# Kernel optimization log

Hardware: AMD Instinct MI355X
Metric: run time of the kernel (lower is better)

Reference implementation:

```python
import jax, jax.numpy as jnp
import numpy as np

N = 50000      # nodes
E = 800000     # edges
IN = 128       # in_dim
H = 64         # h_dim
OUT = 64       # out_dim
R = 5          # num_relations
TB = 12        # 4 * BINS


def setup_inputs() -> dict:
    key = jax.random.key(0)
    ks = jax.random.split(key, 20)
    x = jax.random.normal(ks[0], (N, IN), jnp.float32)
    edge_index = jax.random.randint(ks[1], (2, E), 0, N)
    edge_type = jax.random.randint(ks[2], (E,), 0, R)
    edge_time = jax.random.uniform(ks[3], (E, TB), jnp.float32)
    # xavier_normal on (1,1) -> std 1; on (12,1) -> std sqrt(2/13)
    lambda_sym = jax.random.normal(ks[4], (), jnp.float32)
    beta = jax.random.normal(ks[5], (TB, 1), jnp.float32) * np.float32(np.sqrt(2.0 / (TB + 1)))
    def lin(k, fan_in, fan_out):
        kw, kb = jax.random.split(k)
        bound = 1.0 / np.sqrt(fan_in)
        W = jax.random.uniform(kw, (fan_in, fan_out), jnp.float32, -bound, bound)
        b = jax.random.uniform(kb, (fan_out,), jnp.float32, -bound, bound)
        return W, b
    field_W, field_b = lin(ks[6], IN, H)
    r1 = [lin(k, 2 * H, H) for k in jax.random.split(ks[7], R)]
    r2 = [lin(k, 2 * H, H) for k in jax.random.split(ks[8], R)]
    rel1_W = jnp.stack([w for w, _ in r1]); rel1_b = jnp.stack([b for _, b in r1])
    rel2_W = jnp.stack([w for w, _ in r2]); rel2_b = jnp.stack([b for _, b in r2])
    out0_W, out0_b = lin(ks[9], H, OUT)
    out1_W, out1_b = lin(ks[10], H, OUT)
    out2_W, out2_b = lin(ks[11], H, OUT)
    return {"x": x, "edge_index": edge_index, "edge_type": edge_type, "edge_time": edge_time,
            "lambda_sym": lambda_sym, "beta": beta, "field_W": field_W, "field_b": field_b,
            "rel1_W": rel1_W, "rel1_b": rel1_b, "rel2_W": rel2_W, "rel2_b": rel2_b,
            "out0_W": out0_W, "out0_b": out0_b, "out1_W": out1_W, "out1_b": out1_b,
            "out2_W": out2_W, "out2_b": out2_b}


def _geo_layer(x_emb, src, dst, edge_type, edge_time, lambda_sym, beta, relW, relb):
    # PyG source_to_target: x_j = x[src], x_i = x[dst]; sum-aggregate into dst.
    x_j = x_emb[src]                       # [E, H] gather
    x_i = x_emb[dst]                       # [E, H] gather
    edge_x = jnp.concatenate([x_j, x_i], axis=-1)  # [E, 2H]
    # logit = sum of 4 blockwise dot-products == edge_time @ beta
    logit = (edge_time @ beta)[:, 0]       # [E]
    w = lambda_sym * jnp.exp(-logit)       # [E] time-decay weight
    # relation-specific linear, selected by edge_type (masks partition edges)
    msg = jnp.zeros((edge_x.shape[0], relW.shape[-1]), dtype=x_emb.dtype)
    for r in range(R):
        mask = (edge_type == r)[:, None]
        msg = msg + jnp.where(mask, edge_x @ relW[r] + relb[r], 0.0)
    msg = w[:, None] * msg
    return jax.ops.segment_sum(msg, dst, num_segments=x_emb.shape[0])


def reference(x, edge_index, edge_type, edge_time, lambda_sym, beta,
              field_W, field_b, rel1_W, rel1_b, rel2_W, rel2_b,
              out0_W, out0_b, out1_W, out1_b, out2_W, out2_b):
    src, dst = edge_index[0], edge_index[1]
    e0 = x @ field_W + field_b
    e1 = _geo_layer(e0, src, dst, edge_type, edge_time, lambda_sym, beta, rel1_W, rel1_b)
    e2 = _geo_layer(e1, src, dst, edge_type, edge_time, lambda_sym, beta, rel2_W, rel2_b)
    lr = jax.nn.leaky_relu  # negative_slope 0.01, same as torch default
    return lr(e2 @ out2_W + out2_b) + lr(e1 @ out1_W + out1_b) + lr(e0 @ out0_W + out0_b)
```

## Files before the change

### kernel.cpp

```cpp
#include <hip/hip_runtime.h>
#include <cstdint>
#include <cstddef>

#define NN 50000
#define NE 800000
#define RREL 5
#define NR (NN * RREL)
#define NB5 ((NR + 255) / 256)

typedef __attribute__((ext_vector_type(8))) short short8;
typedef __attribute__((ext_vector_type(4))) float f32x4;
typedef unsigned short ushort_t;

static __device__ __forceinline__ float lrelu(float v) { return v > 0.f ? v : 0.01f * v; }

static __device__ __forceinline__ unsigned short f32_bf16_rn(float x) {
    unsigned u = __float_as_uint(x);
    return (unsigned short)((u + 0x7FFFu + ((u >> 16) & 1u)) >> 16);
}
static __device__ __forceinline__ float bf16_f32(unsigned short h) {
    return __uint_as_float(((unsigned)h) << 16);
}

static __device__ __forceinline__ void split8v(float4 q0, float4 q1, short8& hi, short8& lo) {
    float v[8] = {q0.x, q0.y, q0.z, q0.w, q1.x, q1.y, q1.z, q1.w};
    #pragma unroll
    for (int j = 0; j < 8; ++j) {
        unsigned short h = f32_bf16_rn(v[j]);
        float hf = __uint_as_float(((unsigned)h) << 16);
        unsigned short l = f32_bf16_rn(v[j] - hf);
        hi[j] = (short)h; lo[j] = (short)l;
    }
}

static __device__ __forceinline__ short8 zero8() {
    short8 z = {0, 0, 0, 0, 0, 0, 0, 0};
    return z;
}

__launch_bounds__(256)
__global__ void zero_deg5(int4* __restrict__ p, int n4)
{
    int i = blockIdx.x * 256 + threadIdx.x;
    int stride = gridDim.x * 256;
    for (; i < n4; i += stride)
        p[i] = make_int4(0, 0, 0, 0);
}

__launch_bounds__(512)
__global__ void lin_mfma(const float* __restrict__ X,
                         const short8* __restrict__ ff,
                         const float* __restrict__ bias,
                         ushort_t* __restrict__ Cb, int M)
{
    __shared__ short8 wl[16 * 64];

    const int t = threadIdx.x;
    const int wid = t >> 6, lane = t & 63;
    const int lc = lane & 15, lg = lane >> 4;
    const int row0 = blockIdx.x * 128 + wid * 16;

    const int nA = row0 + lc;
    const bool okA = (nA < M);
    const int nodeA = okA ? nA : 0;

    wl[t] = ff[t];
    wl[t + 512] = ff[t + 512];

    short8 ah[4], al[4];
    #pragma unroll
    for (int s = 0; s < 4; ++s) {
        const float* p = &X[(size_t)nodeA * 128 + s * 32 + lg * 8];
        float4 q0 = okA ? *(const float4*)p       : make_float4(0,0,0,0);
        float4 q1 = okA ? *(const float4*)(p + 4) : make_float4(0,0,0,0);
        split8v(q0, q1, ah[s], al[s]);
    }
    __syncthreads();

    f32x4 acc[4];
    #pragma unroll
    for (int nf = 0; nf < 4; ++nf) acc[nf] = (f32x4){0.f, 0.f, 0.f, 0.f};

    #pragma unroll
    for (int s = 0; s < 4; ++s)
        #pragma unroll
        for (int nf = 0; nf < 4; ++nf) {
            short8 bh = wl[(s * 4 + nf) * 64 + lane];
            acc[nf] = __builtin_amdgcn_mfma_f32_16x16x32_bf16(ah[s], bh, acc[nf], 0, 0, 0);
            acc[nf] = __builtin_amdgcn_mfma_f32_16x16x32_bf16(al[s], bh, acc[nf], 0, 0, 0);
        }

    float bb[4];
    #pragma unroll
    for (int nf = 0; nf < 4; ++nf) bb[nf] = bias[nf * 16 + lc];

    #pragma unroll
    for (int i = 0; i < 4; ++i) {
        int nd = row0 + lg * 4 + i;
        if (nd >= M) continue;
        #pragma unroll
        for (int nf = 0; nf < 4; ++nf)
            Cb[(size_t)nd * 64 + nf * 16 + lc] = f32_bf16_rn(acc[nf][i] + bb[nf]);
    }
}

__launch_bounds__(512)
__global__ void head_mfma(const ushort_t* __restrict__ E0, const ushort_t* __restrict__ E1,
                          const ushort_t* __restrict__ E2,
                          const short8* __restrict__ hf,
                          const float* __restrict__ b0, const float* __restrict__ b1,
                          const float* __restrict__ b2,
                          float* __restrict__ out, int M)
{
    __shared__ short8 wl[24 * 64];

    const int t = threadIdx.x;
    const int wid = t >> 6, lane = t & 63;
    const int lc = lane & 15, lg = lane >> 4;
    const int row0 = blockIdx.x * 128 + wid * 16;

    const int nA = row0 + lc;
    const bool okA = (nA < M);
    const int nodeA = okA ? nA : 0;

    wl[t] = hf[t];
    wl[t + 512] = hf[t + 512];
    wl[t + 1024] = hf[t + 1024];

    const ushort_t* Es[3] = {E0, E1, E2};
    const float* bs[3] = {b0, b1, b2};

    float facc[4][4] = {};
    __syncthreads();

    #pragma unroll
    for (int src = 0; src < 3; ++src) {
        short8 ah[2];
        #pragma unroll
        for (int s = 0; s < 2; ++s) {
            const ushort_t* p = &Es[src][(size_t)nodeA * 64 + s * 32 + lg * 8];
            ah[s] = okA ? *(const short8*)p : zero8();
        }
        f32x4 acc[4];
        #pragma unroll
        for (int nf = 0; nf < 4; ++nf) acc[nf] = (f32x4){0.f, 0.f, 0.f, 0.f};
        #pragma unroll
        for (int s = 0; s < 2; ++s)
            #pragma unroll
            for (int nf = 0; nf < 4; ++nf) {
                short8 bh = wl[((src * 2 + s) * 4 + nf) * 64 + lane];
                acc[nf] = __builtin_amdgcn_mfma_f32_16x16x32_bf16(ah[s], bh, acc[nf], 0, 0, 0);
            }
        float bb[4];
        #pragma unroll
        for (int nf = 0; nf < 4; ++nf) bb[nf] = bs[src][nf * 16 + lc];
        #pragma unroll
        for (int nf = 0; nf < 4; ++nf)
            #pragma unroll
            for (int i = 0; i < 4; ++i)
                facc[nf][i] += lrelu(acc[nf][i] + bb[nf]);
    }

    #pragma unroll
    for (int i = 0; i < 4; ++i) {
        int nd = row0 + lg * 4 + i;
        if (nd >= M) continue;
        #pragma unroll
        for (int nf = 0; nf < 4; ++nf)
            out[(size_t)nd * 64 + nf * 16 + lc] = facc[nf][i];
    }
}

__launch_bounds__(256)
__global__ void zgather(const int* __restrict__ offs5,
                        const unsigned long long* __restrict__ epack,
                        const ushort_t* __restrict__ Eb,
                        ushort_t* __restrict__ Zb16, float* __restrict__ S)
{
    int wid = (blockIdx.x * 256 + threadIdx.x) >> 6;
    int lane = threadIdx.x & 63;
    if (wid >= NN) return;
    const int b = wid * RREL;

    int p    = __builtin_amdgcn_readfirstlane(offs5[b]);
    int n1   = __builtin_amdgcn_readfirstlane(offs5[b + 1]);
    int n2   = __builtin_amdgcn_readfirstlane(offs5[b + 2]);
    int n3   = __builtin_amdgcn_readfirstlane(offs5[b + 3]);
    int n4   = __builtin_amdgcn_readfirstlane(offs5[b + 4]);
    int pend = __builtin_amdgcn_readfirstlane(offs5[b + 5]);

    ushort_t* zr = Zb16 + (size_t)wid * 320 + lane;
    const int INFP = 0x7fffffff;

    int r = 0;
    float zA = 0.f, zB = 0.f, zC = 0.f, zD = 0.f;
    float sA = 0.f, sB = 0.f, sC = 0.f, sD = 0.f;

#define WVAL(q) __uint_as_float((unsigned)((q) >> 32))
#define SRCI(q) ((unsigned)(q) & 0xFFFFFFFFu)

#define FLUSH_CHECK(pe)                                                     \
    while (r < 4 && (pe) == n1) {                                           \
        zr[(size_t)(r << 6)] = f32_bf16_rn(zA + zB + zC + zD);              \
        if (lane == 0) S[b + r] = sA + sB + sC + sD;                        \
        zA = zB = zC = zD = 0.f; sA = sB = sC = sD = 0.f;                   \
        ++r; n1 = n2; n2 = n3; n3 = n4; n4 = INFP;                          \
    }

    for (; p + 8 <= pend; p += 8) {
        unsigned long long q0 = epack[p + 0];
        unsigned long long q1 = epack[p + 1];
        unsigned long long q2 = epack[p + 2];
        unsigned long long q3 = epack[p + 3];
        unsigned long long q4 = epack[p + 4];
        unsigned long long q5 = epack[p + 5];
        unsigned long long q6 = epack[p + 6];
        unsigned long long q7 = epack[p + 7];
        float v0 = bf16_f32(Eb[(size_t)SRCI(q0) * 64 + lane]);
        float v1 = bf16_f32(Eb[(size_t)SRCI(q1) * 64 + lane]);
        float v2 = bf16_f32(Eb[(size_t)SRCI(q2) * 64 + lane]);
        float v3 = bf16_f32(Eb[(size_t)SRCI(q3) * 64 + lane]);
        float v4 = bf16_f32(Eb[(size_t)SRCI(q4) * 64 + lane]);
        float v5 = bf16_f32(Eb[(size_t)SRCI(q5) * 64 + lane]);
        float v6 = bf16_f32(Eb[(size_t)SRCI(q6) * 64 + lane]);
        float v7 = bf16_f32(Eb[(size_t)SRCI(q7) * 64 + lane]);

        FLUSH_CHECK(p + 0);
        zA = fmaf(WVAL(q0), v0, zA); sA += WVAL(q0);
        FLUSH_CHECK(p + 1);
        zB = fmaf(WVAL(q1), v1, zB); sB += WVAL(q1);
        FLUSH_CHECK(p + 2);
        zC = fmaf(WVAL(q2), v2, zC); sC += WVAL(q2);
        FLUSH_CHECK(p + 3);
        zD = fmaf(WVAL(q3), v3, zD); sD += WVAL(q3);
        FLUSH_CHECK(p + 4);
        zA = fmaf(WVAL(q4), v4, zA); sA += WVAL(q4);
        FLUSH_CHECK(p + 5);
        zB = fmaf(WVAL(q5), v5, zB); sB += WVAL(q5);
        FLUSH_CHECK(p + 6);
        zC = fmaf(WVAL(q6), v6, zC); sC += WVAL(q6);
        FLUSH_CHECK(p + 7);
        zD = fmaf(WVAL(q7), v7, zD); sD += WVAL(q7);
    }
    for (; p < pend; ++p) {
        unsigned long long q = epack[p];
        float v = bf16_f32(Eb[(size_t)SRCI(q) * 64 + lane]);
        FLUSH_CHECK(p);
        zA = fmaf(WVAL(q), v, zA);
        sA += WVAL(q);
    }
    while (r < RREL) {
        zr[(size_t)(r << 6)] = f32_bf16_rn(zA + zB + zC + zD);
        if (lane == 0) S[b + r] = sA + sB + sC + sD;
        zA = zB = zC = zD = 0.f; sA = sB = sC = sD = 0.f;
        ++r;
    }
#undef FLUSH_CHECK
#undef WVAL
#undef SRCI
}

__launch_bounds__(256)
__global__ void prep_wfrag(const float* __restrict__ rel1_W, const float* __restrict__ rel2_W,
                           const float* __restrict__ field_W,
                           const float* __restrict__ out0_W, const float* __restrict__ out1_W,
                           const float* __restrict__ out2_W,
                           short8* __restrict__ wf1, short8* __restrict__ wf2,
                           short8* __restrict__ ff, short8* __restrict__ hf)
{
    int bid = blockIdx.x;
    int t = threadIdx.x;

    if (bid < 20) {
        int layer = bid / 10, c = bid % 10;
        const float* relW = layer ? rel2_W : rel1_W;
        short8* wf = layer ? wf2 : wf1;
        for (int sl = t; sl < 512; sl += 256) {
            int rid = sl >> 6, lane = sl & 63;
            int s = rid >> 2, nf = rid & 3;
            int g = lane >> 4, lc = lane & 15;
            int r = (c < 5) ? c : c - 5;
            const float* W = relW + (size_t)r * 8192 + ((c < 5) ? 0 : 4096);
            float v[8];
            #pragma unroll
            for (int j = 0; j < 8; ++j)
                v[j] = W[(size_t)(s * 32 + g * 8 + j) * 64 + nf * 16 + lc];
            float4 q0 = make_float4(v[0], v[1], v[2], v[3]);
            float4 q1 = make_float4(v[4], v[5], v[6], v[7]);
            short8 hi, lo;
            split8v(q0, q1, hi, lo);
            size_t slot = (size_t)c * 1024 + (size_t)((s * 4 + nf) * 64 + lane) * 2;
            wf[slot]     = hi;
            wf[slot + 1] = lo;
        }
    } else if (bid < 24) {
        int s = bid - 20;
        for (int sl = t; sl < 256; sl += 256) {
            int nf = sl >> 6, lane = sl & 63;
            int g = lane >> 4, lc = lane & 15;
            float v[8];
            #pragma unroll
            for (int j = 0; j < 8; ++j)
                v[j] = field_W[(size_t)(s * 32 + g * 8 + j) * 64 + nf * 16 + lc];
            short8 hi;
            #pragma unroll
            for (int j = 0; j < 8; ++j) hi[j] = (short)f32_bf16_rn(v[j]);
            ff[(size_t)(s * 4 + nf) * 64 + lane] = hi;
        }
    } else {
        int hsrc = bid - 24;
        const float* W = (hsrc == 0) ? out0_W : (hsrc == 1) ? out1_W : out2_W;
        for (int sl = t; sl < 512; sl += 256) {
            int rid = sl >> 6, lane = sl & 63;
            int s = rid >> 2, nf = rid & 3;
            if (s >= 2) continue;
            int g = lane >> 4, lc = lane & 15;
            float v[8];
            #pragma unroll
            for (int j = 0; j < 8; ++j)
                v[j] = W[(size_t)(s * 32 + g * 8 + j) * 64 + nf * 16 + lc];
            short8 hi;
            #pragma unroll
            for (int j = 0; j < 8; ++j) hi[j] = (short)f32_bf16_rn(v[j]);
            hf[(size_t)((hsrc * 2 + s) * 4 + nf) * 64 + lane] = hi;
        }
    }
}

__launch_bounds__(512)
__global__ void zgemm_mfma(const ushort_t* __restrict__ Zb16,
                           const ushort_t* __restrict__ EbPrev,
                           const short8* __restrict__ wf,
                           const float* __restrict__ relb,
                           const float* __restrict__ S,
                           ushort_t* __restrict__ Enb, int M)
{
    __shared__ short8 wlds[2][1024];

    const int t = threadIdx.x;
    const int wid = t >> 6, lane = t & 63;
    const int lc = lane & 15, lg = lane >> 4;
    const int row0 = blockIdx.x * 128 + wid * 16;

    const int nA = row0 + lc;
    const bool okA = (nA < M);
    const int nodeA = okA ? nA : 0;

    const int sq = t >> 6, sl = t & 63;
    const int wrA = (sq * 2 + 0) * 64 + sl;
    const int wrB = (sq * 2 + 1) * 64 + sl;

    short8 eh[2];
    #pragma unroll
    for (int s = 0; s < 2; ++s) {
        const ushort_t* p = &EbPrev[(size_t)nodeA * 64 + s * 32 + lg * 8];
        eh[s] = okA ? *(const short8*)p : zero8();
    }

    float sD[4][RREL];
    #pragma unroll
    for (int i = 0; i < 4; ++i) {
        int nd = row0 + lg * 4 + i;
        int ns = (nd < M) ? nd : 0;
        #pragma unroll
        for (int r = 0; r < RREL; ++r)
            sD[i][r] = S[(size_t)ns * RREL + r];
    }

    {
        const short8* wp = wf + (size_t)t * 2;
        short8 sa = wp[0], sb = wp[1];
        wlds[0][wrA] = sa; wlds[0][wrB] = sb;
    }
    short8 az0, az1;
    {
        const ushort_t* zb = &Zb16[(size_t)nodeA * 320 + lg * 8];
        az0 = okA ? *(const short8*)(zb)      : zero8();
        az1 = okA ? *(const short8*)(zb + 32) : zero8();
    }
    __syncthreads();

    f32x4 acc[4];
    #pragma unroll
    for (int nf = 0; nf < 4; ++nf) acc[nf] = (f32x4){0.f, 0.f, 0.f, 0.f};

    short8 sreg_a, sreg_b;
    short8 pz0, pz1;

    #pragma unroll
    for (int c = 0; c < 10; ++c) {
        const int cb = c & 1;
        if (c < 9) {
            const short8* wp = wf + (size_t)(c + 1) * 1024 + (size_t)t * 2;
            sreg_a = wp[0]; sreg_b = wp[1];
        }
        if (c < 4) {
            const ushort_t* zb = &Zb16[(size_t)nodeA * 320 + (c + 1) * 64 + lg * 8];
            pz0 = okA ? *(const short8*)(zb)      : zero8();
            pz1 = okA ? *(const short8*)(zb + 32) : zero8();
        }

        if (c < 5) {
            #pragma unroll
            for (int s = 0; s < 2; ++s) {
                short8 Az = (s == 0) ? az0 : az1;
                #pragma unroll
                for (int nf = 0; nf < 4; ++nf) {
                    short8 bh = wlds[cb][((s * 4 + nf) * 2 + 0) * 64 + lane];
                    short8 bl = wlds[cb][((s * 4 + nf) * 2 + 1) * 64 + lane];
                    acc[nf] = __builtin_amdgcn_mfma_f32_16x16x32_bf16(Az, bh, acc[nf], 0, 0, 0);
                    acc[nf] = __builtin_amdgcn_mfma_f32_16x16x32_bf16(Az, bl, acc[nf], 0, 0, 0);
                }
            }
        } else {
            f32x4 tmp[4];
            #pragma unroll
            for (int nf = 0; nf < 4; ++nf) tmp[nf] = (f32x4){0.f, 0.f, 0.f, 0.f};
            #pragma unroll
            for (int s = 0; s < 2; ++s)
                #pragma unroll
                for (int nf = 0; nf < 4; ++nf) {
                    short8 bh = wlds[cb][((s * 4 + nf) * 2 + 0) * 64 + lane];
                    short8 bl = wlds[cb][((s * 4 + nf) * 2 + 1) * 64 + lane];
                    tmp[nf] = __builtin_amdgcn_mfma_f32_16x16x32_bf16(eh[s], bh, tmp[nf], 0, 0, 0);
                    tmp[nf] = __builtin_amdgcn_mfma_f32_16x16x32_bf16(eh[s], bl, tmp[nf], 0, 0, 0);
                }
            const int r = c - 5;
            #pragma unroll
            for (int nf = 0; nf < 4; ++nf)
                #pragma unroll
                for (int i = 0; i < 4; ++i)
                    acc[nf][i] += sD[i][r] * tmp[nf][i];
        }

        if (c < 4) { az0 = pz0; az1 = pz1; }

        if (c < 9) {
            __syncthreads();
            wlds[cb ^ 1][wrA] = sreg_a;
            wlds[cb ^ 1][wrB] = sreg_b;
            __syncthreads();
        }
    }

    float bbv[4][RREL];
    #pragma unroll
    for (int nf = 0; nf < 4; ++nf)
        #pragma unroll
        for (int r = 0; r < RREL; ++r)
            bbv[nf][r] = relb[r * 64 + nf * 16 + lc];

    #pragma unroll
    for (int i = 0; i < 4; ++i) {
        int nd = row0 + lg * 4 + i;
        if (nd >= M) continue;
        #pragma unroll
        for (int nf = 0; nf < 4; ++nf) {
            float v = acc[nf][i];
            #pragma unroll
            for (int r = 0; r < RREL; ++r)
                v += sD[i][r] * bbv[nf][r];
            Enb[(size_t)nd * 64 + nf * 16 + lc] = f32_bf16_rn(v);
        }
    }
}

__launch_bounds__(256)
__global__ void deg5_hist(const int* __restrict__ dst, const int* __restrict__ etype,
                          int* __restrict__ deg5, int* __restrict__ slot5)
{
    int e = blockIdx.x * 256 + threadIdx.x;
    if (e < NE) slot5[e] = atomicAdd(&deg5[dst[e] * RREL + etype[e]], 1);
}

__launch_bounds__(256)
__global__ void b1_reduce(const int* __restrict__ deg5, int* __restrict__ b1)
{
    __shared__ int sh[256];
    int i = blockIdx.x * 256 + threadIdx.x;
    sh[threadIdx.x] = (i < NR) ? deg5[i] : 0;
    __syncthreads();
    for (int s = 128; s > 0; s >>= 1) {
        if (threadIdx.x < s) sh[threadIdx.x] += sh[threadIdx.x + s];
        __syncthreads();
    }
    if (threadIdx.x == 0) b1[blockIdx.x] = sh[0];
}

__launch_bounds__(256)
__global__ void scan_seq(int* __restrict__ b1, int n)
{
    __shared__ int sh[256];
    __shared__ int carry;
    if (threadIdx.x == 0) carry = 0;
    __syncthreads();
    for (int base = 0; base < n; base += 256) {
        int i = base + threadIdx.x;
        int v = (i < n) ? b1[i] : 0;
        sh[threadIdx.x] = v;
        __syncthreads();
        for (int off = 1; off < 256; off <<= 1) {
            int x = (threadIdx.x >= off) ? sh[threadIdx.x - off] : 0;
            __syncthreads();
            sh[threadIdx.x] += x;
            __syncthreads();
        }
        int excl = sh[threadIdx.x] - v + carry;
        if (i < n) b1[i] = excl;
        __syncthreads();
        if (threadIdx.x == 255) carry = excl + v;
        __syncthreads();
    }
}

__launch_bounds__(256)
__global__ void offs5_final(const int* __restrict__ deg5, const int* __restrict__ b1,
                            int* __restrict__ offs5)
{
    __shared__ int sh[256];
    int t = threadIdx.x;
    int i = blockIdx.x * 256 + t;
    int v = (i < NR) ? deg5[i] : 0;
    sh[t] = v;
    __syncthreads();
    for (int off = 1; off < 256; off <<= 1) {
        int x = (t >= off) ? sh[t - off] : 0;
        __syncthreads();
        sh[t] += x;
        __syncthreads();
    }
    int excl = sh[t] - v + b1[blockIdx.x];
    if (i <= NR) offs5[i] = excl;
}

__launch_bounds__(256)
__global__ void scatter_pass(const int* __restrict__ src, const int* __restrict__ dst,
                             const int* __restrict__ etype,
                             const float* __restrict__ etime,
                             const float* __restrict__ beta,
                             const float* __restrict__ lambda_p,
                             const int* __restrict__ slot5, const int* __restrict__ offs5,
                             unsigned long long* __restrict__ epack)
{
    int e = blockIdx.x * 256 + threadIdx.x;
    if (e >= NE) return;
    float b[12];
    #pragma unroll
    for (int j = 0; j < 12; ++j) b[j] = beta[j];
    const float* et = etime + (size_t)e * 12;
    float4 v0 = *(const float4*)(et);
    float4 v1 = *(const float4*)(et + 4);
    float4 v2 = *(const float4*)(et + 8);
    float logit = v0.x*b[0] + v0.y*b[1] + v0.z*b[2] + v0.w*b[3]
                + v1.x*b[4] + v1.y*b[5] + v1.z*b[6] + v1.w*b[7]
                + v2.x*b[8] + v2.y*b[9] + v2.z*b[10] + v2.w*b[11];
    float we = lambda_p[0] * expf(-logit);
    int p = offs5[dst[e] * RREL + etype[e]] + slot5[e];
    epack[p] = ((unsigned long long)__float_as_uint(we) << 32) | (unsigned)src[e];
}

extern "C" void kernel_launch(void* const* d_in, const int* in_sizes, int n_in,
                              void* d_out, int out_size, void* d_ws, size_t ws_size,
                              hipStream_t stream)
{
    const float* x        = (const float*)d_in[0];
    const int*   eidx     = (const int*)d_in[1];
    const int*   etype    = (const int*)d_in[2];
    const float* etime    = (const float*)d_in[3];
    const float* lambda_p = (const float*)d_in[4];
    const float* beta     = (const float*)d_in[5];
    const float* field_W  = (const float*)d_in[6];
    const float* field_b  = (const float*)d_in[7];
    const float* rel1_W   = (const float*)d_in[8];
    const float* rel1_b   = (const float*)d_in[9];
    const float* rel2_W   = (const float*)d_in[10];
    const float* rel2_b   = (const float*)d_in[11];
    const float* out0_W   = (const float*)d_in[12];
    const float* out0_b   = (const float*)d_in[13];
    const float* out1_W   = (const float*)d_in[14];
    const float* out1_b   = (const float*)d_in[15];
    const float* out2_W   = (const float*)d_in[16];
    const float* out2_b   = (const float*)d_in[17];
    const int* src = eidx;
    const int* dst = eidx + NE;
    float* out = (float*)d_out;

    char* wsb = (char*)d_ws;
    size_t off = 0;
    auto carve = [&](size_t bytes) -> void* {
        void* p = (void*)(wsb + off);
        off += (bytes + 255) & ~(size_t)255;
        return p;
    };
    int*   deg5   = (int*)carve((size_t)NR * 4);
    int*   offs5  = (int*)carve((size_t)(NR + 1) * 4);
    int*   b1     = (int*)carve((size_t)NB5 * 4);
    int*   slot5  = (int*)carve((size_t)NE * 4);
    float* S      = (float*)carve((size_t)NR * 4);
    unsigned long long* epack = (unsigned long long*)carve((size_t)NE * 8);
    ushort_t* e0b = (ushort_t*)carve((size_t)NN * 64 * 2);
    ushort_t* e1b = (ushort_t*)carve((size_t)NN * 64 * 2);
    ushort_t* e2b = (ushort_t*)carve((size_t)NN * 64 * 2);
    ushort_t* Zb16 = (ushort_t*)carve((size_t)NN * 320 * 2);
    short8* wf1   = (short8*)carve((size_t)20 * 16384);
    short8* wf2   = (short8*)carve((size_t)20 * 16384);
    short8* ff    = (short8*)carve((size_t)16 * 64 * 16);
    short8* hf    = (short8*)carve((size_t)24 * 64 * 16);

    dim3 blk(256);
    const int NT128 = (NN + 127) / 128;
    const int EB = (NE + 255) / 256;
    const int GB = (NN * 64 + 255) / 256;

    zero_deg5<<<256, blk, 0, stream>>>((int4*)deg5, (NR + 3) / 4);
    deg5_hist<<<EB, blk, 0, stream>>>(dst, etype, deg5, slot5);
    prep_wfrag<<<27, blk, 0, stream>>>(rel1_W, rel2_W, field_W, out0_W, out1_W, out2_W,
                                       wf1, wf2, ff, hf);
    b1_reduce<<<NB5, blk, 0, stream>>>(deg5, b1);
    scan_seq<<<1, blk, 0, stream>>>(b1, NB5);
    offs5_final<<<NB5, blk, 0, stream>>>(deg5, b1, offs5);
    scatter_pass<<<EB, blk, 0, stream>>>(src, dst, etype, etime, beta, lambda_p,
                                         slot5, offs5, epack);

    lin_mfma<<<dim3(NT128), dim3(512), 0, stream>>>(x, ff, field_b, e0b, NN);

    zgather<<<GB, blk, 0, stream>>>(offs5, epack, e0b, Zb16, S);
    zgemm_mfma<<<dim3(NT128), dim3(512), 0, stream>>>(Zb16, e0b, wf1, rel1_b, S, e1b, NN);

    zgather<<<GB, blk, 0, stream>>>(offs5, epack, e1b, Zb16, S);
    zgemm_mfma<<<dim3(NT128), dim3(512), 0, stream>>>(Zb16, e1b, wf2, rel2_b, S, e2b, NN);

    head_mfma<<<dim3(NT128), dim3(512), 0, stream>>>(e0b, e1b, e2b, hf,
                                                     out0_b, out1_b, out2_b, out, NN);
}
```

Measured before the change: 204.0 us.

## Process two edges per wave in zgather with half-wave bf16x2 gathers

Each (node, relation) segment in the CSR is padded to an even length, and the pad slot is filled with a zero-weight dummy edge. zgather can then have each 32-lane half-wave handle a different edge, reading a packed bf16 pair per lane as a 32-bit load. Partial sums from the two halves are combined with a cross-half shuffle before the store. This halves the loop iterations and makes the row gathers wider. The cost is extra shuffles at every flush, somewhat more padded edges, and a changed scan and offset layout.

```diff
diff --git a/kernel.cpp b/kernel.cpp
--- a/kernel.cpp
+++ b/kernel.cpp
@@ -7,6 +7,7 @@
 #define RREL 5
 #define NR (NN * RREL)
 #define NB5 ((NR + 255) / 256)
+#define NEPAD (NE + NR)
 
 typedef __attribute__((ext_vector_type(8))) short short8;
 typedef __attribute__((ext_vector_type(4))) float f32x4;
@@ -181,6 +182,8 @@
     int lane = threadIdx.x & 63;
     if (wid >= NN) return;
     const int b = wid * RREL;
+    const int h = lane >> 5;
+    const int fl = lane & 31;
 
     int p    = __builtin_amdgcn_readfirstlane(offs5[b]);
     int n1   = __builtin_amdgcn_readfirstlane(offs5[b + 1]);
@@ -189,75 +192,71 @@
     int n4   = __builtin_amdgcn_readfirstlane(offs5[b + 4]);
     int pend = __builtin_amdgcn_readfirstlane(offs5[b + 5]);
 
-    ushort_t* zr = Zb16 + (size_t)wid * 320 + lane;
+    const unsigned* Ebu = (const unsigned*)Eb;
+    unsigned* Zu = (unsigned*)Zb16;
     const int INFP = 0x7fffffff;
 
     int r = 0;
-    float zA = 0.f, zB = 0.f, zC = 0.f, zD = 0.f;
-    float sA = 0.f, sB = 0.f, sC = 0.f, sD = 0.f;
-
-#define WVAL(q) __uint_as_float((unsigned)((q) >> 32))
-#define SRCI(q) ((unsigned)(q) & 0xFFFFFFFFu)
+    float z0 = 0.f, z1 = 0.f, sw = 0.f;
 
 #define FLUSH_CHECK(pe)                                                     \
     while (r < 4 && (pe) == n1) {                                           \
-        zr[(size_t)(r << 6)] = f32_bf16_rn(zA + zB + zC + zD);              \
-        if (lane == 0) S[b + r] = sA + sB + sC + sD;                        \
-        zA = zB = zC = zD = 0.f; sA = sB = sC = sD = 0.f;                   \
+        float o0 = z0 + __shfl_xor(z0, 32);                                 \
+        float o1 = z1 + __shfl_xor(z1, 32);                                 \
+        float os = sw + __shfl_xor(sw, 32);                                 \
+        if (h == 0)                                                         \
+            Zu[(size_t)(b + r) * 32 + fl] =                                 \
+                ((unsigned)f32_bf16_rn(o1) << 16) | f32_bf16_rn(o0);        \
+        if (lane == 0) S[b + r] = os;                                       \
+        z0 = z1 = sw = 0.f;                                                 \
         ++r; n1 = n2; n2 = n3; n3 = n4; n4 = INFP;                          \
     }
 
+#define DO_PAIR(q)                                                          \
+    {                                                                       \
+        unsigned srcn = (unsigned)(q);                                      \
+        float w = __uint_as_float((unsigned)((q) >> 32));                   \
+        unsigned fv = Ebu[(size_t)srcn * 32 + fl];                          \
+        float flo = __uint_as_float(fv << 16);                              \
+        float fhi = __uint_as_float(fv & 0xFFFF0000u);                      \
+        z0 = fmaf(w, flo, z0);                                              \
+        z1 = fmaf(w, fhi, z1);                                              \
+        sw += w;                                                            \
+    }
+
     for (; p + 8 <= pend; p += 8) {
-        unsigned long long q0 = epack[p + 0];
-        unsigned long long q1 = epack[p + 1];
-        unsigned long long q2 = epack[p + 2];
-        unsigned long long q3 = epack[p + 3];
-        unsigned long long q4 = epack[p + 4];
-        unsigned long long q5 = epack[p + 5];
-        unsigned long long q6 = epack[p + 6];
-        unsigned long long q7 = epack[p + 7];
-        float v0 = bf16_f32(Eb[(size_t)SRCI(q0) * 64 + lane]);
-        float v1 = bf16_f32(Eb[(size_t)SRCI(q1) * 64 + lane]);
-        float v2 = bf16_f32(Eb[(size_t)SRCI(q2) * 64 + lane]);
-        float v3 = bf16_f32(Eb[(size_t)SRCI(q3) * 64 + lane]);
-        float v4 = bf16_f32(Eb[(size_t)SRCI(q4) * 64 + lane]);
-        float v5 = bf16_f32(Eb[(size_t)SRCI(q5) * 64 + lane]);
-        float v6 = bf16_f32(Eb[(size_t)SRCI(q6) * 64 + lane]);
-        float v7 = bf16_f32(Eb[(size_t)SRCI(q7) * 64 + lane]);
+        unsigned long long q0 = epack[p + 0 + h];
+        unsigned long long q1 = epack[p + 2 + h];
+        unsigned long long q2 = epack[p + 4 + h];
+        unsigned long long q3 = epack[p + 6 + h];
 
         FLUSH_CHECK(p + 0);
-        zA = fmaf(WVAL(q0), v0, zA); sA += WVAL(q0);
-        FLUSH_CHECK(p + 1);
-        zB = fmaf(WVAL(q1), v1, zB); sB += WVAL(q1);
+        DO_PAIR(q0);
         FLUSH_CHECK(p + 2);
-        zC = fmaf(WVAL(q2), v2, zC); sC += WVAL(q2);
-        FLUSH_CHECK(p + 3);
-        zD = fmaf(WVAL(q3), v3, zD); sD += WVAL(q3);
+        DO_PAIR(q1);
         FLUSH_CHECK(p + 4);
-        zA = fmaf(WVAL(q4), v4, zA); sA += WVAL(q4);
-        FLUSH_CHECK(p + 5);
-        zB = fmaf(WVAL(q5), v5, zB); sB += WVAL(q5);
+        DO_PAIR(q2);
         FLUSH_CHECK(p + 6);
-        zC = fmaf(WVAL(q6), v6, zC); sC += WVAL(q6);
-        FLUSH_CHECK(p + 7);
-        zD = fmaf(WVAL(q7), v7, zD); sD += WVAL(q7);
-    }
-    for (; p < pend; ++p) {
-        unsigned long long q = epack[p];
-        float v = bf16_f32(Eb[(size_t)SRCI(q) * 64 + lane]);
+        DO_PAIR(q3);
+    }
+    for (; p < pend; p += 2) {
+        unsigned long long q = epack[p + h];
         FLUSH_CHECK(p);
-        zA = fmaf(WVAL(q), v, zA);
-        sA += WVAL(q);
+        DO_PAIR(q);
     }
     while (r < RREL) {
-        zr[(size_t)(r << 6)] = f32_bf16_rn(zA + zB + zC + zD);
-        if (lane == 0) S[b + r] = sA + sB + sC + sD;
-        zA = zB = zC = zD = 0.f; sA = sB = sC = sD = 0.f;
+        float o0 = z0 + __shfl_xor(z0, 32);
+        float o1 = z1 + __shfl_xor(z1, 32);
+        float os = sw + __shfl_xor(sw, 32);
+        if (h == 0)
+            Zu[(size_t)(b + r) * 32 + fl] =
+                ((unsigned)f32_bf16_rn(o1) << 16) | f32_bf16_rn(o0);
+        if (lane == 0) S[b + r] = os;
+        z0 = z1 = sw = 0.f;
         ++r;
     }
 #undef FLUSH_CHECK
-#undef WVAL
-#undef SRCI
+#undef DO_PAIR
 }
 
 __launch_bounds__(256)
@@ -478,7 +477,8 @@
 {
     __shared__ int sh[256];
     int i = blockIdx.x * 256 + threadIdx.x;
-    sh[threadIdx.x] = (i < NR) ? deg5[i] : 0;
+    int d = (i < NR) ? deg5[i] : 0;
+    sh[threadIdx.x] = (d + 1) & ~1;
     __syncthreads();
     for (int s = 128; s > 0; s >>= 1) {
         if (threadIdx.x < s) sh[threadIdx.x] += sh[threadIdx.x + s];
@@ -515,12 +515,13 @@
 
 __launch_bounds__(256)
 __global__ void offs5_final(const int* __restrict__ deg5, const int* __restrict__ b1,
-                            int* __restrict__ offs5)
+                            int* __restrict__ offs5, unsigned long long* __restrict__ epack)
 {
     __shared__ int sh[256];
     int t = threadIdx.x;
     int i = blockIdx.x * 256 + t;
-    int v = (i < NR) ? deg5[i] : 0;
+    int d = (i < NR) ? deg5[i] : 0;
+    int v = (d + 1) & ~1;
     sh[t] = v;
     __syncthreads();
     for (int off = 1; off < 256; off <<= 1) {
@@ -531,6 +532,7 @@
     }
     int excl = sh[t] - v + b1[blockIdx.x];
     if (i <= NR) offs5[i] = excl;
+    if (i < NR && (d & 1)) epack[excl + d] = 0ULL;
 }
 
 __launch_bounds__(256)
@@ -597,7 +599,7 @@
     int*   b1     = (int*)carve((size_t)NB5 * 4);
     int*   slot5  = (int*)carve((size_t)NE * 4);
     float* S      = (float*)carve((size_t)NR * 4);
-    unsigned long long* epack = (unsigned long long*)carve((size_t)NE * 8);
+    unsigned long long* epack = (unsigned long long*)carve((size_t)NEPAD * 8);
     ushort_t* e0b = (ushort_t*)carve((size_t)NN * 64 * 2);
     ushort_t* e1b = (ushort_t*)carve((size_t)NN * 64 * 2);
     ushort_t* e2b = (ushort_t*)carve((size_t)NN * 64 * 2);
@@ -618,7 +620,7 @@
                                        wf1, wf2, ff, hf);
     b1_reduce<<<NB5, blk, 0, stream>>>(deg5, b1);
     scan_seq<<<1, blk, 0, stream>>>(b1, NB5);
-    offs5_final<<<NB5, blk, 0, stream>>>(deg5, b1, offs5);
+    offs5_final<<<NB5, blk, 0, stream>>>(deg5, b1, offs5, epack);
     scatter_pass<<<EB, blk, 0, stream>>>(src, dst, etype, etime, beta, lambda_p,
                                          slot5, offs5, epack);
 
```

Result: slower. 223.8 us (+9.7%).

## Process two nodes per wavefront in zgather with packed bf16x2 loads

Applied to the files above, without the earlier changes.

Each wavefront now handles two destination nodes, with each half-wave of 32 lanes loading a 32-bit word (two bf16 features) per gathered row instead of one 16-bit value per lane. This halves the number of wavefronts and widens the per-lane gather loads, reducing load instruction count and per-edge overhead. Per-node offsets are no longer wave-uniform (readfirstlane removed), so control flow in the flush loop can diverge between the two halves. Fewer independent accumulators per feature may add some FMA latency.

```diff
diff --git a/kernel.cpp b/kernel.cpp
--- a/kernel.cpp
+++ b/kernel.cpp
@@ -177,34 +177,54 @@
                         const ushort_t* __restrict__ Eb,
                         ushort_t* __restrict__ Zb16, float* __restrict__ S)
 {
-    int wid = (blockIdx.x * 256 + threadIdx.x) >> 6;
+    int gw = (blockIdx.x * 256 + threadIdx.x) >> 6;
     int lane = threadIdx.x & 63;
-    if (wid >= NN) return;
-    const int b = wid * RREL;
-
-    int p    = __builtin_amdgcn_readfirstlane(offs5[b]);
-    int n1   = __builtin_amdgcn_readfirstlane(offs5[b + 1]);
-    int n2   = __builtin_amdgcn_readfirstlane(offs5[b + 2]);
-    int n3   = __builtin_amdgcn_readfirstlane(offs5[b + 3]);
-    int n4   = __builtin_amdgcn_readfirstlane(offs5[b + 4]);
-    int pend = __builtin_amdgcn_readfirstlane(offs5[b + 5]);
-
-    ushort_t* zr = Zb16 + (size_t)wid * 320 + lane;
+    const int h = lane >> 5;
+    const int fl = lane & 31;
+    int node = gw * 2 + h;
+    if (node >= NN) return;
+    const int b = node * RREL;
+
+    int p    = offs5[b];
+    int n1   = offs5[b + 1];
+    int n2   = offs5[b + 2];
+    int n3   = offs5[b + 3];
+    int n4   = offs5[b + 4];
+    int pend = offs5[b + 5];
+
+    const unsigned* Ebu = (const unsigned*)Eb;
+    unsigned* Zu = (unsigned*)Zb16;
     const int INFP = 0x7fffffff;
 
     int r = 0;
-    float zA = 0.f, zB = 0.f, zC = 0.f, zD = 0.f;
-    float sA = 0.f, sB = 0.f, sC = 0.f, sD = 0.f;
-
+    float zA0 = 0.f, zA1 = 0.f, zB0 = 0.f, zB1 = 0.f;
+    float swA = 0.f, swB = 0.f;
+
+#define SRCI(q) ((unsigned)(q))
 #define WVAL(q) __uint_as_float((unsigned)((q) >> 32))
-#define SRCI(q) ((unsigned)(q) & 0xFFFFFFFFu)
 
 #define FLUSH_CHECK(pe)                                                     \
     while (r < 4 && (pe) == n1) {                                           \
-        zr[(size_t)(r << 6)] = f32_bf16_rn(zA + zB + zC + zD);              \
-        if (lane == 0) S[b + r] = sA + sB + sC + sD;                        \
-        zA = zB = zC = zD = 0.f; sA = sB = sC = sD = 0.f;                   \
+        Zu[(size_t)(b + r) * 32 + fl] =                                     \
+            ((unsigned)f32_bf16_rn(zA1 + zB1) << 16) | f32_bf16_rn(zA0 + zB0); \
+        if (fl == 0) S[b + r] = swA + swB;                                  \
+        zA0 = zA1 = zB0 = zB1 = 0.f; swA = swB = 0.f;                       \
         ++r; n1 = n2; n2 = n3; n3 = n4; n4 = INFP;                          \
+    }
+
+#define ACC_A(q, fv)                                                        \
+    {                                                                       \
+        float w = WVAL(q);                                                  \
+        zA0 = fmaf(w, __uint_as_float((fv) << 16), zA0);                    \
+        zA1 = fmaf(w, __uint_as_float((fv) & 0xFFFF0000u), zA1);            \
+        swA += w;                                                           \
+    }
+#define ACC_B(q, fv)                                                        \
+    {                                                                       \
+        float w = WVAL(q);                                                  \
+        zB0 = fmaf(w, __uint_as_float((fv) << 16), zB0);                    \
+        zB1 = fmaf(w, __uint_as_float((fv) & 0xFFFF0000u), zB1);            \
+        swB += w;                                                           \
     }
 
     for (; p + 8 <= pend; p += 8) {
@@ -216,48 +236,42 @@
         unsigned long long q5 = epack[p + 5];
         unsigned long long q6 = epack[p + 6];
         unsigned long long q7 = epack[p + 7];
-        float v0 = bf16_f32(Eb[(size_t)SRCI(q0) * 64 + lane]);
-        float v1 = bf16_f32(Eb[(size_t)SRCI(q1) * 64 + lane]);
-        float v2 = bf16_f32(Eb[(size_t)SRCI(q2) * 64 + lane]);
-        float v3 = bf16_f32(Eb[(size_t)SRCI(q3) * 64 + lane]);
-        float v4 = bf16_f32(Eb[(size_t)SRCI(q4) * 64 + lane]);
-        float v5 = bf16_f32(Eb[(size_t)SRCI(q5) * 64 + lane]);
-        float v6 = bf16_f32(Eb[(size_t)SRCI(q6) * 64 + lane]);
-        float v7 = bf16_f32(Eb[(size_t)SRCI(q7) * 64 + lane]);
-
-        FLUSH_CHECK(p + 0);
-        zA = fmaf(WVAL(q0), v0, zA); sA += WVAL(q0);
-        FLUSH_CHECK(p + 1);
-        zB = fmaf(WVAL(q1), v1, zB); sB += WVAL(q1);
-        FLUSH_CHECK(p + 2);
-        zC = fmaf(WVAL(q2), v2, zC); sC += WVAL(q2);
-        FLUSH_CHECK(p + 3);
-        zD = fmaf(WVAL(q3), v3, zD); sD += WVAL(q3);
-        FLUSH_CHECK(p + 4);
-        zA = fmaf(WVAL(q4), v4, zA); sA += WVAL(q4);
-        FLUSH_CHECK(p + 5);
-        zB = fmaf(WVAL(q5), v5, zB); sB += WVAL(q5);
-        FLUSH_CHECK(p + 6);
-        zC = fmaf(WVAL(q6), v6, zC); sC += WVAL(q6);
-        FLUSH_CHECK(p + 7);
-        zD = fmaf(WVAL(q7), v7, zD); sD += WVAL(q7);
+        unsigned f0 = Ebu[(size_t)SRCI(q0) * 32 + fl];
+        unsigned f1 = Ebu[(size_t)SRCI(q1) * 32 + fl];
+        unsigned f2 = Ebu[(size_t)SRCI(q2) * 32 + fl];
+        unsigned f3 = Ebu[(size_t)SRCI(q3) * 32 + fl];
+        unsigned f4 = Ebu[(size_t)SRCI(q4) * 32 + fl];
+        unsigned f5 = Ebu[(size_t)SRCI(q5) * 32 + fl];
+        unsigned f6 = Ebu[(size_t)SRCI(q6) * 32 + fl];
+        unsigned f7 = Ebu[(size_t)SRCI(q7) * 32 + fl];
+
+        FLUSH_CHECK(p + 0); ACC_A(q0, f0);
+        FLUSH_CHECK(p + 1); ACC_B(q1, f1);
+        FLUSH_CHECK(p + 2); ACC_A(q2, f2);
+        FLUSH_CHECK(p + 3); ACC_B(q3, f3);
+        FLUSH_CHECK(p + 4); ACC_A(q4, f4);
+        FLUSH_CHECK(p + 5); ACC_B(q5, f5);
+        FLUSH_CHECK(p + 6); ACC_A(q6, f6);
+        FLUSH_CHECK(p + 7); ACC_B(q7, f7);
     }
     for (; p < pend; ++p) {
         unsigned long long q = epack[p];
-        float v = bf16_f32(Eb[(size_t)SRCI(q) * 64 + lane]);
+        unsigned fv = Ebu[(size_t)SRCI(q) * 32 + fl];
         FLUSH_CHECK(p);
-        zA = fmaf(WVAL(q), v, zA);
-        sA += WVAL(q);
+        ACC_A(q, fv);
     }
     while (r < RREL) {
-        zr[(size_t)(r << 6)] = f32_bf16_rn(zA + zB + zC + zD);
-        if (lane == 0) S[b + r] = sA + sB + sC + sD;
-        zA = zB = zC = zD = 0.f; sA = sB = sC = sD = 0.f;
+        Zu[(size_t)(b + r) * 32 + fl] =
+            ((unsigned)f32_bf16_rn(zA1 + zB1) << 16) | f32_bf16_rn(zA0 + zB0);
+        if (fl == 0) S[b + r] = swA + swB;
+        zA0 = zA1 = zB0 = zB1 = 0.f; swA = swB = 0.f;
         ++r;
     }
 #undef FLUSH_CHECK
+#undef ACC_A
+#undef ACC_B
+#undef SRCI
 #undef WVAL
-#undef SRCI
 }
 
 __launch_bounds__(256)
@@ -610,7 +624,7 @@
     dim3 blk(256);
     const int NT128 = (NN + 127) / 128;
     const int EB = (NE + 255) / 256;
-    const int GB = (NN * 64 + 255) / 256;
+    const int GB2 = (((NN + 1) / 2) * 64 + 255) / 256;
 
     zero_deg5<<<256, blk, 0, stream>>>((int4*)deg5, (NR + 3) / 4);
     deg5_hist<<<EB, blk, 0, stream>>>(dst, etype, deg5, slot5);
@@ -624,10 +638,10 @@
 
     lin_mfma<<<dim3(NT128), dim3(512), 0, stream>>>(x, ff, field_b, e0b, NN);
 
-    zgather<<<GB, blk, 0, stream>>>(offs5, epack, e0b, Zb16, S);
+    zgather<<<GB2, blk, 0, stream>>>(offs5, epack, e0b, Zb16, S);
     zgemm_mfma<<<dim3(NT128), dim3(512), 0, stream>>>(Zb16, e0b, wf1, rel1_b, S, e1b, NN);
 
-    zgather<<<GB, blk, 0, stream>>>(offs5, epack, e1b, Zb16, S);
+    zgather<<<GB2, blk, 0, stream>>>(offs5, epack, e1b, Zb16, S);
     zgemm_mfma<<<dim3(NT128), dim3(512), 0, stream>>>(Zb16, e1b, wf2, rel2_b, S, e2b, NN);
 
     head_mfma<<<dim3(NT128), dim3(512), 0, stream>>>(e0b, e1b, e2b, hf,
```

Measured after the change: 203.2 us, median of 2. About the same (-0.4%).

## Pack segment-end markers into edge records and gather four nodes per wavefront

Applied to the files above, without the earlier changes.

The scatter pass now encodes, in spare bits of each packed edge record, a flag marking the last edge of its (node, relation) segment and the segment's index within a group of four nodes. The gather kernel gives each wavefront four consecutive nodes (20 segments) and flushes on the marker bit instead of comparing positions against offsets. This removes the per-edge offset comparisons and gives each wave a longer run of edges. In exchange it uses a single accumulator chain, so there is less instruction-level parallelism in the FMAs, launches a quarter of the waves, and relies on source indices fitting in 17 bits.

```diff
diff --git a/kernel.cpp b/kernel.cpp
--- a/kernel.cpp
+++ b/kernel.cpp
@@ -177,34 +177,36 @@
                         const ushort_t* __restrict__ Eb,
                         ushort_t* __restrict__ Zb16, float* __restrict__ S)
 {
-    int wid = (blockIdx.x * 256 + threadIdx.x) >> 6;
+    int gw = (blockIdx.x * 256 + threadIdx.x) >> 6;
     int lane = threadIdx.x & 63;
-    if (wid >= NN) return;
-    const int b = wid * RREL;
-
-    int p    = __builtin_amdgcn_readfirstlane(offs5[b]);
-    int n1   = __builtin_amdgcn_readfirstlane(offs5[b + 1]);
-    int n2   = __builtin_amdgcn_readfirstlane(offs5[b + 2]);
-    int n3   = __builtin_amdgcn_readfirstlane(offs5[b + 3]);
-    int n4   = __builtin_amdgcn_readfirstlane(offs5[b + 4]);
-    int pend = __builtin_amdgcn_readfirstlane(offs5[b + 5]);
-
-    ushort_t* zr = Zb16 + (size_t)wid * 320 + lane;
-    const int INFP = 0x7fffffff;
-
-    int r = 0;
-    float zA = 0.f, zB = 0.f, zC = 0.f, zD = 0.f;
-    float sA = 0.f, sB = 0.f, sC = 0.f, sD = 0.f;
-
-#define WVAL(q) __uint_as_float((unsigned)((q) >> 32))
-#define SRCI(q) ((unsigned)(q) & 0xFFFFFFFFu)
-
-#define FLUSH_CHECK(pe)                                                     \
-    while (r < 4 && (pe) == n1) {                                           \
-        zr[(size_t)(r << 6)] = f32_bf16_rn(zA + zB + zC + zD);              \
-        if (lane == 0) S[b + r] = sA + sB + sC + sD;                        \
-        zA = zB = zC = zD = 0.f; sA = sB = sC = sD = 0.f;                   \
-        ++r; n1 = n2; n2 = n3; n3 = n4; n4 = INFP;                          \
+    int nbase = gw * 4;
+    if (nbase >= NN) return;
+    const int bstart = nbase * RREL;
+    const int bcount = (NR - bstart < 4 * RREL) ? (NR - bstart) : (4 * RREL);
+
+    int p    = offs5[bstart];
+    int pend = offs5[bstart + bcount];
+
+    float z = 0.f, sw = 0.f;
+    int lastf = -1;
+
+#define WVAL(q64) __uint_as_float((unsigned)((q64) >> 32))
+
+#define STEP(q64, v)                                                        \
+    {                                                                       \
+        unsigned lo = (unsigned)(q64);                                      \
+        float w = WVAL(q64);                                                \
+        z = fmaf(w, v, z); sw += w;                                         \
+        if (lo & (1u << 22)) {                                              \
+            int rs = (int)((lo >> 17) & 31u);                               \
+            for (int j = lastf + 1; j < rs; ++j) {                          \
+                Zb16[(size_t)(bstart + j) * 64 + lane] = 0;                 \
+                if (lane == 0) S[bstart + j] = 0.f;                         \
+            }                                                               \
+            Zb16[(size_t)(bstart + rs) * 64 + lane] = f32_bf16_rn(z);       \
+            if (lane == 0) S[bstart + rs] = sw;                             \
+            z = 0.f; sw = 0.f; lastf = rs;                                  \
+        }                                                                   \
     }
 
     for (; p + 8 <= pend; p += 8) {
@@ -216,48 +218,35 @@
         unsigned long long q5 = epack[p + 5];
         unsigned long long q6 = epack[p + 6];
         unsigned long long q7 = epack[p + 7];
-        float v0 = bf16_f32(Eb[(size_t)SRCI(q0) * 64 + lane]);
-        float v1 = bf16_f32(Eb[(size_t)SRCI(q1) * 64 + lane]);
-        float v2 = bf16_f32(Eb[(size_t)SRCI(q2) * 64 + lane]);
-        float v3 = bf16_f32(Eb[(size_t)SRCI(q3) * 64 + lane]);
-        float v4 = bf16_f32(Eb[(size_t)SRCI(q4) * 64 + lane]);
-        float v5 = bf16_f32(Eb[(size_t)SRCI(q5) * 64 + lane]);
-        float v6 = bf16_f32(Eb[(size_t)SRCI(q6) * 64 + lane]);
-        float v7 = bf16_f32(Eb[(size_t)SRCI(q7) * 64 + lane]);
-
-        FLUSH_CHECK(p + 0);
-        zA = fmaf(WVAL(q0), v0, zA); sA += WVAL(q0);
-        FLUSH_CHECK(p + 1);
-        zB = fmaf(WVAL(q1), v1, zB); sB += WVAL(q1);
-        FLUSH_CHECK(p + 2);
-        zC = fmaf(WVAL(q2), v2, zC); sC += WVAL(q2);
-        FLUSH_CHECK(p + 3);
-        zD = fmaf(WVAL(q3), v3, zD); sD += WVAL(q3);
-        FLUSH_CHECK(p + 4);
-        zA = fmaf(WVAL(q4), v4, zA); sA += WVAL(q4);
-        FLUSH_CHECK(p + 5);
-        zB = fmaf(WVAL(q5), v5, zB); sB += WVAL(q5);
-        FLUSH_CHECK(p + 6);
-        zC = fmaf(WVAL(q6), v6, zC); sC += WVAL(q6);
-        FLUSH_CHECK(p + 7);
-        zD = fmaf(WVAL(q7), v7, zD); sD += WVAL(q7);
+        float v0 = bf16_f32(Eb[(size_t)((unsigned)q0 & 0x1FFFFu) * 64 + lane]);
+        float v1 = bf16_f32(Eb[(size_t)((unsigned)q1 & 0x1FFFFu) * 64 + lane]);
+        float v2 = bf16_f32(Eb[(size_t)((unsigned)q2 & 0x1FFFFu) * 64 + lane]);
+        float v3 = bf16_f32(Eb[(size_t)((unsigned)q3 & 0x1FFFFu) * 64 + lane]);
+        float v4 = bf16_f32(Eb[(size_t)((unsigned)q4 & 0x1FFFFu) * 64 + lane]);
+        float v5 = bf16_f32(Eb[(size_t)((unsigned)q5 & 0x1FFFFu) * 64 + lane]);
+        float v6 = bf16_f32(Eb[(size_t)((unsigned)q6 & 0x1FFFFu) * 64 + lane]);
+        float v7 = bf16_f32(Eb[(size_t)((unsigned)q7 & 0x1FFFFu) * 64 + lane]);
+
+        STEP(q0, v0);
+        STEP(q1, v1);
+        STEP(q2, v2);
+        STEP(q3, v3);
+        STEP(q4, v4);
+        STEP(q5, v5);
+        STEP(q6, v6);
+        STEP(q7, v7);
     }
     for (; p < pend; ++p) {
         unsigned long long q = epack[p];
-        float v = bf16_f32(Eb[(size_t)SRCI(q) * 64 + lane]);
-        FLUSH_CHECK(p);
-        zA = fmaf(WVAL(q), v, zA);
-        sA += WVAL(q);
-    }
-    while (r < RREL) {
-        zr[(size_t)(r << 6)] = f32_bf16_rn(zA + zB + zC + zD);
-        if (lane == 0) S[b + r] = sA + sB + sC + sD;
-        zA = zB = zC = zD = 0.f; sA = sB = sC = sD = 0.f;
-        ++r;
-    }
-#undef FLUSH_CHECK
+        float v = bf16_f32(Eb[(size_t)((unsigned)q & 0x1FFFFu) * 64 + lane]);
+        STEP(q, v);
+    }
+    for (int j = lastf + 1; j < bcount; ++j) {
+        Zb16[(size_t)(bstart + j) * 64 + lane] = 0;
+        if (lane == 0) S[bstart + j] = 0.f;
+    }
+#undef STEP
 #undef WVAL
-#undef SRCI
 }
 
 __launch_bounds__(256)
@@ -540,6 +529,7 @@
                              const float* __restrict__ beta,
                              const float* __restrict__ lambda_p,
                              const int* __restrict__ slot5, const int* __restrict__ offs5,
+                             const int* __restrict__ deg5,
                              unsigned long long* __restrict__ epack)
 {
     int e = blockIdx.x * 256 + threadIdx.x;
@@ -555,8 +545,14 @@
                 + v1.x*b[4] + v1.y*b[5] + v1.z*b[6] + v1.w*b[7]
                 + v2.x*b[8] + v2.y*b[9] + v2.z*b[10] + v2.w*b[11];
     float we = lambda_p[0] * expf(-logit);
-    int p = offs5[dst[e] * RREL + etype[e]] + slot5[e];
-    epack[p] = ((unsigned long long)__float_as_uint(we) << 32) | (unsigned)src[e];
+    int d = dst[e], r = etype[e];
+    int key = d * RREL + r;
+    int sl = slot5[e];
+    unsigned marker = (sl + 1 == deg5[key]) ? (1u << 22) : 0u;
+    unsigned relseg = (unsigned)((d & 3) * RREL + r) << 17;
+    unsigned lo = (unsigned)src[e] | relseg | marker;
+    int p = offs5[key] + sl;
+    epack[p] = ((unsigned long long)__float_as_uint(we) << 32) | lo;
 }
 
 extern "C" void kernel_launch(void* const* d_in, const int* in_sizes, int n_in,
@@ -610,7 +606,8 @@
     dim3 blk(256);
     const int NT128 = (NN + 127) / 128;
     const int EB = (NE + 255) / 256;
-    const int GB = (NN * 64 + 255) / 256;
+    const int NW4 = (NN + 3) / 4;
+    const int GB4 = (NW4 * 64 + 255) / 256;
 
     zero_deg5<<<256, blk, 0, stream>>>((int4*)deg5, (NR + 3) / 4);
     deg5_hist<<<EB, blk, 0, stream>>>(dst, etype, deg5, slot5);
@@ -620,14 +617,14 @@
     scan_seq<<<1, blk, 0, stream>>>(b1, NB5);
     offs5_final<<<NB5, blk, 0, stream>>>(deg5, b1, offs5);
     scatter_pass<<<EB, blk, 0, stream>>>(src, dst, etype, etime, beta, lambda_p,
-                                         slot5, offs5, epack);
+                                         slot5, offs5, deg5, epack);
 
     lin_mfma<<<dim3(NT128), dim3(512), 0, stream>>>(x, ff, field_b, e0b, NN);
 
-    zgather<<<GB, blk, 0, stream>>>(offs5, epack, e0b, Zb16, S);
+    zgather<<<GB4, blk, 0, stream>>>(offs5, epack, e0b, Zb16, S);
     zgemm_mfma<<<dim3(NT128), dim3(512), 0, stream>>>(Zb16, e0b, wf1, rel1_b, S, e1b, NN);
 
-    zgather<<<GB, blk, 0, stream>>>(offs5, epack, e1b, Zb16, S);
+    zgather<<<GB4, blk, 0, stream>>>(offs5, epack, e1b, Zb16, S);
     zgemm_mfma<<<dim3(NT128), dim3(512), 0, stream>>>(Zb16, e1b, wf2, rel2_b, S, e2b, NN);
 
     head_mfma<<<dim3(NT128), dim3(512), 0, stream>>>(e0b, e1b, e2b, hf,
```

Result: slower. 209.5 us (+2.7%).
